# Kernel optimization log

Hardware: AMD Instinct MI355X
Metric: run time of the kernel (lower is better)

Reference implementation:

```python
import jax, jax.numpy as jnp
import numpy as np

N_USERS = 8192
D = 128
E = 262144        # known edges (nonzero_idx rows)
K = 131072        # static pad size for data-dependent candidate extraction
COS_THR = 0.3
TAU = 0.2


def setup_inputs() -> dict:
    key = jax.random.key(0)
    k1, k2, k3, k4 = jax.random.split(key, 4)
    user_emb = jax.random.normal(k1, (N_USERS, D), dtype=jnp.float32)
    nonzero_idx = jax.random.randint(k2, (E, 2), 0, N_USERS)
    W = jax.random.normal(k3, (2, 2 * D), dtype=jnp.float32) * 0.05  # mlp_s weight [2, 2*latent]
    b = jnp.zeros((2,), dtype=jnp.float32)                            # mlp_s bias
    gumbel_noise = jax.random.gumbel(k4, (E + K, 2), dtype=jnp.float32)
    return {"user_emb": user_emb, "W": W, "b": b,
            "gumbel_noise": gumbel_noise, "nonzero_idx": nonzero_idx}


def reference(user_emb, W, b, gumbel_noise, nonzero_idx):
    n = user_emb.shape[0]
    # ---- get_candidate_pair ----
    norm = jnp.linalg.norm(user_emb, axis=1, keepdims=True)
    u = user_emb / jnp.maximum(norm, 1e-12)          # F.normalize(dim=1)
    cos = u @ u.T                                    # [n, n]
    diag = jnp.arange(n)
    cos = cos.at[diag, diag].set(-1.0)               # fill_diagonal_(-1)
    cos = cos.at[nonzero_idx[:, 0], nonzero_idx[:, 1]].set(-1.0)
    mask = cos > COS_THR
    # static-size nonzero; padded slots point at (0,0) where cos == -1,
    # so they behave as invalid candidates (weight 0 downstream).
    ci, cj = jnp.nonzero(mask, size=K, fill_value=0)
    cand_vals = cos[ci, cj]                          # padded entries = -1
    cand_idx = jnp.stack([ci, cj], axis=1)           # [K, 2]

    # ---- forward ----
    pair_idx = jnp.concatenate([nonzero_idx, cand_idx], axis=0)   # [E+K, 2]
    u_emb = user_emb[pair_idx[:, 0]]
    v_emb = user_emb[pair_idx[:, 1]]
    concat_emb = jnp.concatenate([u_emb, v_emb], axis=1)          # [E+K, 2D]
    logits = concat_emb @ W.T + b                                 # [E+K, 2]

    # hard gumbel-softmax (straight-through)
    y_soft = jax.nn.softmax((logits + gumbel_noise) / TAU, axis=-1)
    y_hard = jax.nn.one_hot(jnp.argmax(y_soft, axis=-1), 2, dtype=y_soft.dtype)
    gumbel_output = y_hard + y_soft - jax.lax.stop_gradient(y_soft)
    gumbel_retain = gumbel_output[:, 0]                           # [E+K]

    # ---- get_edge_weight ----
    cand_w = jnp.maximum(cand_vals, 0.0)                          # masked_fill(<0, 0)
    weights = jnp.concatenate([jnp.ones((E,), dtype=cand_w.dtype), cand_w])
    w = gumbel_retain * weights                                   # [E+K]
    gumbel_01 = w
    gumbel_retain_w = jnp.concatenate([w[:, None], w[:, None]], axis=0)  # [2(E+K), 1]
    return gumbel_01, gumbel_retain_w, pair_idx
```

## Files before the change

kernel.cpp:

```cpp
#include <hip/hip_runtime.h>
#include <hip/hip_bf16.h>
#include <math.h>

#define N_USERS 8192
#define DIMS    128
#define EDGES   262144
#define KCAND   131072
#define NTOT    (EDGES + KCAND)
#define LISTCAP 131072
#define CAPB    1024
#define NTILES  1056
#define COS_THR 0.3f
#define EPS_SEL 6e-3f
#define LOGIT_MARGIN 2e-3f
#define DEADKEY 0xFFFFFFFFu

typedef short bf16x8 __attribute__((ext_vector_type(8)));
typedef float f32x4  __attribute__((ext_vector_type(4)));


__global__ __launch_bounds__(256) void prep_k(const float* __restrict__ x,
                                              const float* __restrict__ W,
                                              const int* __restrict__ nz,
                                              float* __restrict__ un,
                                              unsigned short* __restrict__ u0,
                                              float4* __restrict__ P,
                                              unsigned* __restrict__ excl) {
  if (blockIdx.x < 256) {
#pragma clang fp contract(off)
    const int tid  = threadIdx.x;
    const int rloc = tid >> 3;
    const int j    = tid & 7;
    const int i    = blockIdx.x * 32 + rloc;
    const float* r = x + (size_t)i * DIMS;

    float vals[16];
    float a = 0.f;
#pragma unroll
    for (int b8 = 0; b8 < 16; ++b8) {
      float t = r[b8 * 8 + j];
      vals[b8] = t;
      a = a + t * t;
    }
    a = a + __shfl_xor(a, 1, 64);
    a = a + __shfl_xor(a, 2, 64);
    float s = a + __shfl_xor(a, 4, 64);
    float n = (float)sqrt((double)s);
    n = fmaxf(n, 1e-12f);

    unsigned short* slab = u0 + (size_t)(i >> 7) * 16384 + (i & 127) * 8;
    float p0 = 0.f, p1 = 0.f, p2 = 0.f, p3 = 0.f;
#pragma unroll
    for (int b8 = 0; b8 < 16; ++b8) {
      int k = b8 * 8 + j;
      float t = vals[b8];
      float v = t / n;
      un[(size_t)i * DIMS + k] = v;
      __hip_bfloat16 h = __float2bfloat16(v);
      slab[(size_t)b8 * 1024 + j] = *(unsigned short*)&h;
      p0 = fmaf(t, W[k], p0);
      p1 = fmaf(t, W[128 + k], p1);
      p2 = fmaf(t, W[256 + k], p2);
      p3 = fmaf(t, W[384 + k], p3);
    }
#pragma unroll
    for (int m = 1; m < 8; m <<= 1) {
      p0 += __shfl_xor(p0, m, 64);
      p1 += __shfl_xor(p1, m, 64);
      p2 += __shfl_xor(p2, m, 64);
      p3 += __shfl_xor(p3, m, 64);
    }
    if (j == 0) P[i] = make_float4(p0, p1, p2, p3);
  } else {
    int t = (blockIdx.x - 256) * 256 + threadIdx.x;
    if (t < EDGES) {
      uint2 e = ((const uint2*)nz)[t];
      atomicOr(&excl[(size_t)e.x * 256 + (e.y >> 5)], 1u << (e.y & 31));
    }
  }
}

__global__ __launch_bounds__(512) void mfma_pass(const unsigned short* __restrict__ u0,
                                                 uint2* __restrict__ list,
                                                 int* __restrict__ gcount) {
  __shared__ uint2 svec[CAPB];
  __shared__ int lcnt, lbase;

  const int tid  = threadIdx.x;
  const int lane = tid & 63;
  const int wv   = tid >> 6;
  const int quad = lane >> 4;
  const int l15  = lane & 15;

  int b = blockIdx.x, cj = 0;
  while ((cj + 1) * (cj + 2) <= b) ++cj;
  const int ri = b - cj * (cj + 1);
  const int I0 = ri * 128, J0 = cj * 256;
  const int moff = (wv & 3) * 32;
  const int nhalf = wv >> 2;
  const int jbase = J0 + nhalf * 128;

  if (tid == 0) lcnt = 0;
  __syncthreads();

  const unsigned short* __restrict__ Abase = u0 + (size_t)ri * 16384;
  const unsigned short* __restrict__ Bbase = u0 + (size_t)(cj * 2 + nhalf) * 16384;

  f32x4 acc[2][8];
#pragma unroll
  for (int mt = 0; mt < 2; ++mt)
#pragma unroll
    for (int nt = 0; nt < 8; ++nt)
#pragma unroll
      for (int g = 0; g < 4; ++g) acc[mt][nt][g] = 0.f;

  bf16x8 a0_0, a0_1, b0_0, b0_1, b0_2, b0_3, b0_4, b0_5, b0_6, b0_7;
  bf16x8 a1_0, a1_1, b1_0, b1_1, b1_2, b1_3, b1_4, b1_5, b1_6, b1_7;

#define LOADF(AN0, AN1, BN0, BN1, BN2, BN3, BN4, BN5, BN6, BN7, KC)           \
  {                                                                           \
    const int cq = (KC) * 4 + quad;                                           \
    AN0 = *(const bf16x8*)&Abase[(size_t)(cq * 128 + moff + l15) * 8];        \
    AN1 = *(const bf16x8*)&Abase[(size_t)(cq * 128 + moff + 16 + l15) * 8];   \
    BN0 = *(const bf16x8*)&Bbase[(size_t)(cq * 128 + 0 * 16 + l15) * 8];      \
    BN1 = *(const bf16x8*)&Bbase[(size_t)(cq * 128 + 1 * 16 + l15) * 8];      \
    BN2 = *(const bf16x8*)&Bbase[(size_t)(cq * 128 + 2 * 16 + l15) * 8];      \
    BN3 = *(const bf16x8*)&Bbase[(size_t)(cq * 128 + 3 * 16 + l15) * 8];      \
    BN4 = *(const bf16x8*)&Bbase[(size_t)(cq * 128 + 4 * 16 + l15) * 8];      \
    BN5 = *(const bf16x8*)&Bbase[(size_t)(cq * 128 + 5 * 16 + l15) * 8];      \
    BN6 = *(const bf16x8*)&Bbase[(size_t)(cq * 128 + 6 * 16 + l15) * 8];      \
    BN7 = *(const bf16x8*)&Bbase[(size_t)(cq * 128 + 7 * 16 + l15) * 8];      \
  }

#define MFMAF(AN0, AN1, BN0, BN1, BN2, BN3, BN4, BN5, BN6, BN7)               \
  {                                                                           \
    acc[0][0] = __builtin_amdgcn_mfma_f32_16x16x32_bf16(AN0, BN0, acc[0][0], 0, 0, 0); \
    acc[0][1] = __builtin_amdgcn_mfma_f32_16x16x32_bf16(AN0, BN1, acc[0][1], 0, 0, 0); \
    acc[0][2] = __builtin_amdgcn_mfma_f32_16x16x32_bf16(AN0, BN2, acc[0][2], 0, 0, 0); \
    acc[0][3] = __builtin_amdgcn_mfma_f32_16x16x32_bf16(AN0, BN3, acc[0][3], 0, 0, 0); \
    acc[0][4] = __builtin_amdgcn_mfma_f32_16x16x32_bf16(AN0, BN4, acc[0][4], 0, 0, 0); \
    acc[0][5] = __builtin_amdgcn_mfma_f32_16x16x32_bf16(AN0, BN5, acc[0][5], 0, 0, 0); \
    acc[0][6] = __builtin_amdgcn_mfma_f32_16x16x32_bf16(AN0, BN6, acc[0][6], 0, 0, 0); \
    acc[0][7] = __builtin_amdgcn_mfma_f32_16x16x32_bf16(AN0, BN7, acc[0][7], 0, 0, 0); \
    acc[1][0] = __builtin_amdgcn_mfma_f32_16x16x32_bf16(AN1, BN0, acc[1][0], 0, 0, 0); \
    acc[1][1] = __builtin_amdgcn_mfma_f32_16x16x32_bf16(AN1, BN1, acc[1][1], 0, 0, 0); \
    acc[1][2] = __builtin_amdgcn_mfma_f32_16x16x32_bf16(AN1, BN2, acc[1][2], 0, 0, 0); \
    acc[1][3] = __builtin_amdgcn_mfma_f32_16x16x32_bf16(AN1, BN3, acc[1][3], 0, 0, 0); \
    acc[1][4] = __builtin_amdgcn_mfma_f32_16x16x32_bf16(AN1, BN4, acc[1][4], 0, 0, 0); \
    acc[1][5] = __builtin_amdgcn_mfma_f32_16x16x32_bf16(AN1, BN5, acc[1][5], 0, 0, 0); \
    acc[1][6] = __builtin_amdgcn_mfma_f32_16x16x32_bf16(AN1, BN6, acc[1][6], 0, 0, 0); \
    acc[1][7] = __builtin_amdgcn_mfma_f32_16x16x32_bf16(AN1, BN7, acc[1][7], 0, 0, 0); \
  }

  LOADF(a0_0, a0_1, b0_0, b0_1, b0_2, b0_3, b0_4, b0_5, b0_6, b0_7, 0)
  LOADF(a1_0, a1_1, b1_0, b1_1, b1_2, b1_3, b1_4, b1_5, b1_6, b1_7, 1)
  MFMAF(a0_0, a0_1, b0_0, b0_1, b0_2, b0_3, b0_4, b0_5, b0_6, b0_7)
  LOADF(a0_0, a0_1, b0_0, b0_1, b0_2, b0_3, b0_4, b0_5, b0_6, b0_7, 2)
  MFMAF(a1_0, a1_1, b1_0, b1_1, b1_2, b1_3, b1_4, b1_5, b1_6, b1_7)
  LOADF(a1_0, a1_1, b1_0, b1_1, b1_2, b1_3, b1_4, b1_5, b1_6, b1_7, 3)
  MFMAF(a0_0, a0_1, b0_0, b0_1, b0_2, b0_3, b0_4, b0_5, b0_6, b0_7)
  MFMAF(a1_0, a1_1, b1_0, b1_1, b1_2, b1_3, b1_4, b1_5, b1_6, b1_7)
#undef LOADF
#undef MFMAF

#pragma unroll
  for (int mt = 0; mt < 2; ++mt)
#pragma unroll
    for (int nt = 0; nt < 8; ++nt)
#pragma unroll
      for (int g = 0; g < 4; ++g) {
        float v = acc[mt][nt][g];
        if (v > COS_THR - EPS_SEL) {
          int i = I0 + moff + mt * 16 + quad * 4 + g;
          int j = jbase + nt * 16 + l15;
          if (j > i) {
            int idx = atomicAdd(&lcnt, 2);
            if (idx + 1 < CAPB) {
              svec[idx]     = make_uint2(((unsigned)i << 13) | j,
                                         __float_as_uint(v));
              svec[idx + 1] = make_uint2(((unsigned)j << 13) | i,
                                         __float_as_uint(v));
            }
          }
        }
      }

  __syncthreads();
  int n = min(lcnt, CAPB);
  if (tid == 0) lbase = atomicAdd(gcount, n);
  __syncthreads();
  int base = lbase;
  for (int t = tid; t < n; t += 512) {
    int o = base + t;
    if (o < LISTCAP) list[o] = svec[t];
  }
}

__global__ __launch_bounds__(256) void resolve_hist_k(const float* __restrict__ un,
                                                      const unsigned* __restrict__ excl,
                                                      uint2* __restrict__ list,
                                                      const int* __restrict__ gcount,
                                                      int* __restrict__ row_cnt) {
  int t = blockIdx.x * 256 + threadIdx.x;
  int n = min(*gcount, LISTCAP);
  if (t >= n) return;
  uint2 e = list[t];
  int i = e.x >> 13, j = e.x & 8191;
  unsigned word = excl[(size_t)i * 256 + (j >> 5)];
  bool alive = !((word >> (j & 31)) & 1u);
  float v = __uint_as_float(e.y);
  if (alive && v <= COS_THR + EPS_SEL) {
    const float* a = un + (size_t)i * DIMS;
    const float* b = un + (size_t)j * DIMS;
    float s = 0.f;
    for (int k = 0; k < DIMS; ++k) s = fmaf(a[k], b[k], s);
    alive = (s > COS_THR);
    if (alive) list[t] = make_uint2(e.x, __float_as_uint(s));
  }
  if (!alive) list[t] = make_uint2(DEADKEY, 0u);
  else        atomicAdd(&row_cnt[i], 1);
}

__global__ __launch_bounds__(256) void scan8k(const int* __restrict__ cnt,
                                              int* __restrict__ off) {
  __shared__ int sm[256];
  int t = threadIdx.x;
  int base = t * 32;
  int s = 0;
  for (int i = 0; i < 32; ++i) s += cnt[base + i];
  sm[t] = s;
  __syncthreads();
  int x = s;
  for (int d = 1; d < 256; d <<= 1) {
    int y = (t >= d) ? sm[t - d] : 0;
    __syncthreads();
    x += y;
    sm[t] = x;
    __syncthreads();
  }
  int run = x - s;
  for (int i = 0; i < 32; ++i) { off[base + i] = run; run += cnt[base + i]; }
  if (t == 255) off[N_USERS] = x;
}

__global__ __launch_bounds__(256) void scatter_k(const uint2* __restrict__ list,
                                                 const int* __restrict__ gcount,
                                                 const int* __restrict__ row_off,
                                                 int* __restrict__ row_pos,
                                                 int* __restrict__ cand_i,
                                                 int* __restrict__ cand_j,
                                                 float* __restrict__ cand_v) {
  int t = blockIdx.x * 256 + threadIdx.x;
  int n = min(*gcount, LISTCAP);
  if (t >= n) return;
  uint2 e = list[t];
  if (e.x == DEADKEY) return;
  int i = e.x >> 13, j = e.x & 8191;
  int pos = row_off[i] + atomicAdd(&row_pos[i], 1);
  if (pos < KCAND) {
    cand_i[pos] = i;
    cand_j[pos] = j;
    cand_v[pos] = __uint_as_float(e.y);
  }
}

__global__ __launch_bounds__(256) void sortrow_k(const int* __restrict__ row_off,
                                                 const int* __restrict__ row_cnt,
                                                 int* __restrict__ cand_j,
                                                 float* __restrict__ cand_v) {
  int r = blockIdx.x * 256 + threadIdx.x;
  if (r >= N_USERS) return;
  int o = row_off[r], c = row_cnt[r];
  if (o + c > KCAND) c = max(0, KCAND - o);
  for (int a = 1; a < c; ++a) {
    int jv = cand_j[o + a];
    float vv = cand_v[o + a];
    int b = a - 1;
    while (b >= 0 && cand_j[o + b] > jv) {
      cand_j[o + b + 1] = cand_j[o + b];
      cand_v[o + b + 1] = cand_v[o + b];
      --b;
    }
    cand_j[o + b + 1] = jv;
    cand_v[o + b + 1] = vv;
  }
}

__global__ __launch_bounds__(256) void finalize_k(const float* __restrict__ ue,
                                                  const float* __restrict__ W,
                                                  const float* __restrict__ b,
                                                  const float* __restrict__ g,
                                                  const int* __restrict__ nz,
                                                  const int* __restrict__ cand_i,
                                                  const int* __restrict__ cand_j,
                                                  const float* __restrict__ cand_v,
                                                  const int* __restrict__ row_off,
                                                  const float4* __restrict__ P,
                                                  float* __restrict__ out) {
  int p = blockIdx.x * 256 + threadIdx.x;
  if (p >= NTOT) return;

  int i, j;
  float wgt;
  if (p < EDGES) {
    i = nz[2 * p];
    j = nz[2 * p + 1];
    wgt = 1.0f;
  } else {
    int q = p - EDGES;
    if (q >= row_off[N_USERS]) {
      out[p] = 0.0f;
      out[NTOT + p] = 0.0f;
      out[2 * NTOT + p] = 0.0f;
      out[3 * NTOT + 2 * p + 0] = 0.0f;
      out[3 * NTOT + 2 * p + 1] = 0.0f;
      return;
    }
    i = cand_i[q];
    j = cand_j[q];
    wgt = fmaxf(cand_v[q], 0.0f);
  }

  float4 Pi = P[i], Pj = P[j];
  float l0 = Pi.x + Pj.y + b[0];
  float l1 = Pi.z + Pj.w + b[1];
  float g0 = g[2 * p], g1 = g[2 * p + 1];
  float s0 = l0 + g0, s1 = l1 + g1;

  if (fabsf(s0 - s1) < LOGIT_MARGIN) {
    const float* ri = ue + (size_t)i * DIMS;
    const float* rj = ue + (size_t)j * DIMS;
    float e0 = 0.f, e1 = 0.f;
    for (int k = 0; k < DIMS; ++k) {
      e0 = fmaf(ri[k], W[k], e0);
      e1 = fmaf(ri[k], W[256 + k], e1);
    }
    for (int k = 0; k < DIMS; ++k) {
      e0 = fmaf(rj[k], W[128 + k], e0);
      e1 = fmaf(rj[k], W[384 + k], e1);
    }
    s0 = (e0 + b[0]) + g0;
    s1 = (e1 + b[1]) + g1;
  }

  float w = (s0 >= s1) ? wgt : 0.0f;

  out[p] = w;
  out[NTOT + p] = w;
  out[2 * NTOT + p] = w;
  out[3 * NTOT + 2 * p + 0] = (float)i;
  out[3 * NTOT + 2 * p + 1] = (float)j;
}

extern "C" void kernel_launch(void* const* d_in, const int* in_sizes, int n_in,
                              void* d_out, int out_size, void* d_ws, size_t ws_size,
                              hipStream_t stream) {
  (void)in_sizes; (void)n_in; (void)out_size; (void)ws_size;

  const float* user_emb = (const float*)d_in[0];
  const float* W        = (const float*)d_in[1];
  const float* b        = (const float*)d_in[2];
  const float* gnoise   = (const float*)d_in[3];
  const int*   nz       = (const int*)d_in[4];
  float* out = (float*)d_out;

  char* ws = (char*)d_ws;
  float*          un      = (float*)(ws + 0);
  unsigned short* u0      = (unsigned short*)(ws + (4u << 20));
  unsigned*       excl    = (unsigned*)(ws + (6u << 20));
  char*           zbase   = ws + (14u << 20);
  int*            gcount  = (int*)(zbase);
  int*            row_cnt = (int*)(zbase + 64);
  int*            row_pos = (int*)(zbase + 64 + 32768);
  int*            row_off = (int*)(ws + (14u << 20) + (96u << 10));
  uint2*          list    = (uint2*)(ws + (15u << 20));
  int*            cand_i  = (int*)(ws + (16u << 20));
  int*            cand_j  = (int*)(ws + (16u << 20) + (512u << 10));
  float*          cand_v  = (float*)(ws + (17u << 20));
  float4*         P       = (float4*)(ws + (17u << 20) + (512u << 10));

  hipMemsetAsync(excl, 0, (8u << 20) + (96u << 10), stream);

  prep_k<<<256 + EDGES / 256, 256, 0, stream>>>(user_emb, W, nz, un, u0, P, excl);
  mfma_pass<<<NTILES, 512, 0, stream>>>(u0, list, gcount);
  resolve_hist_k<<<LISTCAP / 256, 256, 0, stream>>>(un, excl, list, gcount,
                                                    row_cnt);
  scan8k<<<1, 256, 0, stream>>>(row_cnt, row_off);
  scatter_k<<<LISTCAP / 256, 256, 0, stream>>>(list, gcount, row_off, row_pos,
                                               cand_i, cand_j, cand_v);
  sortrow_k<<<N_USERS / 256, 256, 0, stream>>>(row_off, row_cnt, cand_j, cand_v);
  finalize_k<<<NTOT / 256, 256, 0, stream>>>(user_emb, W, b, gnoise, nz,
                                             cand_i, cand_j, cand_v, row_off,
                                             P, out);
}
```

Measured before the change: 148.5 us.

## Fuse candidate resolve into MFMA pass and merge scan/scatter/sort/finalize into one kernel

The exclusion-bitmap check, exact fp32 recheck of near-threshold pairs and per-row counting move into the MFMA tile epilogue, so the separate resolve kernel is gone. Scan, scatter, per-row insertion sort and output emission are merged into a single 256-block tail kernel. Each block redundantly recomputes the global prefix scan over row counts and scans the whole candidate list to pick out its own 32 rows. The goal is fewer launches and fewer global round trips, at the cost of redundant per-block list scans and serialized dot products inside the MFMA epilogue.

```diff
diff --git a/kernel.cpp b/kernel.cpp
--- a/kernel.cpp
+++ b/kernel.cpp
@@ -13,11 +13,17 @@
 #define COS_THR 0.3f
 #define EPS_SEL 6e-3f
 #define LOGIT_MARGIN 2e-3f
-#define DEADKEY 0xFFFFFFFFu
 
 typedef short bf16x8 __attribute__((ext_vector_type(8)));
 typedef float f32x4  __attribute__((ext_vector_type(4)));
 
+
+__attribute__((noinline)) __device__ float exact_dot(const float* __restrict__ a,
+                                                     const float* __restrict__ b) {
+  float s = 0.f;
+  for (int k = 0; k < DIMS; ++k) s = fmaf(a[k], b[k], s);
+  return s;
+}
 
 __global__ __launch_bounds__(256) void prep_k(const float* __restrict__ x,
                                               const float* __restrict__ W,
@@ -81,8 +87,11 @@
 }
 
 __global__ __launch_bounds__(512) void mfma_pass(const unsigned short* __restrict__ u0,
+                                                 const float* __restrict__ un,
+                                                 const unsigned* __restrict__ excl,
                                                  uint2* __restrict__ list,
-                                                 int* __restrict__ gcount) {
+                                                 int* __restrict__ gcount,
+                                                 int* __restrict__ row_cnt) {
   __shared__ uint2 svec[CAPB];
   __shared__ int lcnt, lbase;
 
@@ -174,12 +183,30 @@
           int i = I0 + moff + mt * 16 + quad * 4 + g;
           int j = jbase + nt * 16 + l15;
           if (j > i) {
-            int idx = atomicAdd(&lcnt, 2);
-            if (idx + 1 < CAPB) {
-              svec[idx]     = make_uint2(((unsigned)i << 13) | j,
-                                         __float_as_uint(v));
-              svec[idx + 1] = make_uint2(((unsigned)j << 13) | i,
-                                         __float_as_uint(v));
+            float vv = v;
+            bool pass = true;
+            if (v <= COS_THR + EPS_SEL) {
+              vv = exact_dot(un + (size_t)i * DIMS, un + (size_t)j * DIMS);
+              pass = (vv > COS_THR);
+            }
+            if (pass) {
+              unsigned wij = excl[(size_t)i * 256 + (j >> 5)];
+              unsigned wji = excl[(size_t)j * 256 + (i >> 5)];
+              unsigned uvv = __float_as_uint(vv);
+              if (!((wij >> (j & 31)) & 1u)) {
+                int idx = atomicAdd(&lcnt, 1);
+                if (idx < CAPB) {
+                  svec[idx] = make_uint2(((unsigned)i << 13) | j, uvv);
+                  atomicAdd(&row_cnt[i], 1);
+                }
+              }
+              if (!((wji >> (i & 31)) & 1u)) {
+                int idx = atomicAdd(&lcnt, 1);
+                if (idx < CAPB) {
+                  svec[idx] = make_uint2(((unsigned)j << 13) | i, uvv);
+                  atomicAdd(&row_cnt[j], 1);
+                }
+              }
             }
           }
         }
@@ -196,131 +223,13 @@
   }
 }
 
-__global__ __launch_bounds__(256) void resolve_hist_k(const float* __restrict__ un,
-                                                      const unsigned* __restrict__ excl,
-                                                      uint2* __restrict__ list,
-                                                      const int* __restrict__ gcount,
-                                                      int* __restrict__ row_cnt) {
-  int t = blockIdx.x * 256 + threadIdx.x;
-  int n = min(*gcount, LISTCAP);
-  if (t >= n) return;
-  uint2 e = list[t];
-  int i = e.x >> 13, j = e.x & 8191;
-  unsigned word = excl[(size_t)i * 256 + (j >> 5)];
-  bool alive = !((word >> (j & 31)) & 1u);
-  float v = __uint_as_float(e.y);
-  if (alive && v <= COS_THR + EPS_SEL) {
-    const float* a = un + (size_t)i * DIMS;
-    const float* b = un + (size_t)j * DIMS;
-    float s = 0.f;
-    for (int k = 0; k < DIMS; ++k) s = fmaf(a[k], b[k], s);
-    alive = (s > COS_THR);
-    if (alive) list[t] = make_uint2(e.x, __float_as_uint(s));
-  }
-  if (!alive) list[t] = make_uint2(DEADKEY, 0u);
-  else        atomicAdd(&row_cnt[i], 1);
-}
-
-__global__ __launch_bounds__(256) void scan8k(const int* __restrict__ cnt,
-                                              int* __restrict__ off) {
-  __shared__ int sm[256];
-  int t = threadIdx.x;
-  int base = t * 32;
-  int s = 0;
-  for (int i = 0; i < 32; ++i) s += cnt[base + i];
-  sm[t] = s;
-  __syncthreads();
-  int x = s;
-  for (int d = 1; d < 256; d <<= 1) {
-    int y = (t >= d) ? sm[t - d] : 0;
-    __syncthreads();
-    x += y;
-    sm[t] = x;
-    __syncthreads();
-  }
-  int run = x - s;
-  for (int i = 0; i < 32; ++i) { off[base + i] = run; run += cnt[base + i]; }
-  if (t == 255) off[N_USERS] = x;
-}
-
-__global__ __launch_bounds__(256) void scatter_k(const uint2* __restrict__ list,
-                                                 const int* __restrict__ gcount,
-                                                 const int* __restrict__ row_off,
-                                                 int* __restrict__ row_pos,
-                                                 int* __restrict__ cand_i,
-                                                 int* __restrict__ cand_j,
-                                                 float* __restrict__ cand_v) {
-  int t = blockIdx.x * 256 + threadIdx.x;
-  int n = min(*gcount, LISTCAP);
-  if (t >= n) return;
-  uint2 e = list[t];
-  if (e.x == DEADKEY) return;
-  int i = e.x >> 13, j = e.x & 8191;
-  int pos = row_off[i] + atomicAdd(&row_pos[i], 1);
-  if (pos < KCAND) {
-    cand_i[pos] = i;
-    cand_j[pos] = j;
-    cand_v[pos] = __uint_as_float(e.y);
-  }
-}
-
-__global__ __launch_bounds__(256) void sortrow_k(const int* __restrict__ row_off,
-                                                 const int* __restrict__ row_cnt,
-                                                 int* __restrict__ cand_j,
-                                                 float* __restrict__ cand_v) {
-  int r = blockIdx.x * 256 + threadIdx.x;
-  if (r >= N_USERS) return;
-  int o = row_off[r], c = row_cnt[r];
-  if (o + c > KCAND) c = max(0, KCAND - o);
-  for (int a = 1; a < c; ++a) {
-    int jv = cand_j[o + a];
-    float vv = cand_v[o + a];
-    int b = a - 1;
-    while (b >= 0 && cand_j[o + b] > jv) {
-      cand_j[o + b + 1] = cand_j[o + b];
-      cand_v[o + b + 1] = cand_v[o + b];
-      --b;
-    }
-    cand_j[o + b + 1] = jv;
-    cand_v[o + b + 1] = vv;
-  }
-}
-
-__global__ __launch_bounds__(256) void finalize_k(const float* __restrict__ ue,
-                                                  const float* __restrict__ W,
-                                                  const float* __restrict__ b,
-                                                  const float* __restrict__ g,
-                                                  const int* __restrict__ nz,
-                                                  const int* __restrict__ cand_i,
-                                                  const int* __restrict__ cand_j,
-                                                  const float* __restrict__ cand_v,
-                                                  const int* __restrict__ row_off,
-                                                  const float4* __restrict__ P,
-                                                  float* __restrict__ out) {
-  int p = blockIdx.x * 256 + threadIdx.x;
-  if (p >= NTOT) return;
-
-  int i, j;
-  float wgt;
-  if (p < EDGES) {
-    i = nz[2 * p];
-    j = nz[2 * p + 1];
-    wgt = 1.0f;
-  } else {
-    int q = p - EDGES;
-    if (q >= row_off[N_USERS]) {
-      out[p] = 0.0f;
-      out[NTOT + p] = 0.0f;
-      out[2 * NTOT + p] = 0.0f;
-      out[3 * NTOT + 2 * p + 0] = 0.0f;
-      out[3 * NTOT + 2 * p + 1] = 0.0f;
-      return;
-    }
-    i = cand_i[q];
-    j = cand_j[q];
-    wgt = fmaxf(cand_v[q], 0.0f);
-  }
-
+__device__ __forceinline__ void emit_out(int p, int i, int j, float wgt,
+                                         const float4* __restrict__ P,
+                                         const float* __restrict__ b,
+                                         const float* __restrict__ g,
+                                         const float* __restrict__ ue,
+                                         const float* __restrict__ W,
+                                         float* __restrict__ out) {
   float4 Pi = P[i], Pj = P[j];
   float l0 = Pi.x + Pj.y + b[0];
   float l1 = Pi.z + Pj.w + b[1];
@@ -344,12 +253,121 @@
   }
 
   float w = (s0 >= s1) ? wgt : 0.0f;
-
   out[p] = w;
   out[NTOT + p] = w;
   out[2 * NTOT + p] = w;
   out[3 * NTOT + 2 * p + 0] = (float)i;
   out[3 * NTOT + 2 * p + 1] = (float)j;
+}
+
+__global__ __launch_bounds__(256) void tail_k(const uint2* __restrict__ list,
+                                              const int* __restrict__ gcount,
+                                              const int* __restrict__ row_cnt,
+                                              int* __restrict__ cand_i,
+                                              int* __restrict__ cand_j,
+                                              float* __restrict__ cand_v,
+                                              const float* __restrict__ ue,
+                                              const float* __restrict__ W,
+                                              const float* __restrict__ b,
+                                              const float* __restrict__ g,
+                                              const int* __restrict__ nz,
+                                              const float4* __restrict__ P,
+                                              float* __restrict__ out) {
+  __shared__ int s_chunk[256];
+  __shared__ int s_off[32];
+  __shared__ int s_pos[32];
+  __shared__ int s_lo, s_M;
+
+  const int tid = threadIdx.x;
+  const int bo  = blockIdx.x;
+
+  int s = 0;
+  {
+    const int rb = tid * 32;
+    for (int k = 0; k < 32; ++k) s += row_cnt[rb + k];
+  }
+  s_chunk[tid] = s;
+  __syncthreads();
+  int x = s;
+  for (int d = 1; d < 256; d <<= 1) {
+    int y = (tid >= d) ? s_chunk[tid - d] : 0;
+    __syncthreads();
+    x += y;
+    s_chunk[tid] = x;
+    __syncthreads();
+  }
+  if (tid == 255) s_M = x;
+  if (tid == bo)  s_lo = x - s;
+  __syncthreads();
+  if (tid == 0) {
+    int run = s_lo;
+    for (int k = 0; k < 32; ++k) {
+      s_off[k] = run;
+      run += row_cnt[bo * 32 + k];
+    }
+  }
+  if (tid < 32) s_pos[tid] = 0;
+  __syncthreads();
+
+  const int n = min(*gcount, LISTCAP);
+  const int M = s_M;
+
+  for (int t = tid; t < n; t += 256) {
+    uint2 e = list[t];
+    int i = e.x >> 13;
+    if ((i >> 5) == bo) {
+      int lr = i & 31;
+      int pos = s_off[lr] + atomicAdd(&s_pos[lr], 1);
+      if (pos < KCAND) {
+        cand_i[pos] = i;
+        cand_j[pos] = e.x & 8191;
+        cand_v[pos] = __uint_as_float(e.y);
+      }
+    }
+  }
+  __syncthreads();
+
+  if (tid < 32) {
+    int o = s_off[tid], c = s_pos[tid];
+    if (o + c > KCAND) c = max(0, KCAND - o);
+    for (int a = 1; a < c; ++a) {
+      int jv = cand_j[o + a];
+      float vv = cand_v[o + a];
+      int bq = a - 1;
+      while (bq >= 0 && cand_j[o + bq] > jv) {
+        cand_j[o + bq + 1] = cand_j[o + bq];
+        cand_v[o + bq + 1] = cand_v[o + bq];
+        --bq;
+      }
+      cand_j[o + bq + 1] = jv;
+      cand_v[o + bq + 1] = vv;
+    }
+  }
+  __syncthreads();
+
+  {
+    int lo = s_off[0];
+    int hi = min(s_off[31] + s_pos[31], KCAND);
+    for (int q = lo + tid; q < hi; q += 256) {
+      int ci = cand_i[q], cjj = cand_j[q];
+      float wgt = fmaxf(cand_v[q], 0.0f);
+      emit_out(EDGES + q, ci, cjj, wgt, P, b, g, ue, W, out);
+    }
+  }
+
+  for (int p = bo * 1024 + tid; p < bo * 1024 + 1024; p += 256) {
+    uint2 e = ((const uint2*)nz)[p];
+    emit_out(p, (int)e.x, (int)e.y, 1.0f, P, b, g, ue, W, out);
+  }
+
+  for (int q = M + bo * 256 + tid; q < KCAND; q += 256 * 256) {
+    int p = EDGES + q;
+    out[p] = 0.0f;
+    out[NTOT + p] = 0.0f;
+    out[2 * NTOT + p] = 0.0f;
+    out[3 * NTOT + 2 * p + 0] = 0.0f;
+    out[3 * NTOT + 2 * p + 1] = 0.0f;
+  }
 }
 
 extern "C" void kernel_launch(void* const* d_in, const int* in_sizes, int n_in,
@@ -371,8 +389,6 @@
   char*           zbase   = ws + (14u << 20);
   int*            gcount  = (int*)(zbase);
   int*            row_cnt = (int*)(zbase + 64);
-  int*            row_pos = (int*)(zbase + 64 + 32768);
-  int*            row_off = (int*)(ws + (14u << 20) + (96u << 10));
   uint2*          list    = (uint2*)(ws + (15u << 20));
   int*            cand_i  = (int*)(ws + (16u << 20));
   int*            cand_j  = (int*)(ws + (16u << 20) + (512u << 10));
@@ -382,14 +398,7 @@
   hipMemsetAsync(excl, 0, (8u << 20) + (96u << 10), stream);
 
   prep_k<<<256 + EDGES / 256, 256, 0, stream>>>(user_emb, W, nz, un, u0, P, excl);
-  mfma_pass<<<NTILES, 512, 0, stream>>>(u0, list, gcount);
-  resolve_hist_k<<<LISTCAP / 256, 256, 0, stream>>>(un, excl, list, gcount,
-                                                    row_cnt);
-  scan8k<<<1, 256, 0, stream>>>(row_cnt, row_off);
-  scatter_k<<<LISTCAP / 256, 256, 0, stream>>>(list, gcount, row_off, row_pos,
-                                               cand_i, cand_j, cand_v);
-  sortrow_k<<<N_USERS / 256, 256, 0, stream>>>(row_off, row_cnt, cand_j, cand_v);
-  finalize_k<<<NTOT / 256, 256, 0, stream>>>(user_emb, W, b, gnoise, nz,
-                                             cand_i, cand_j, cand_v, row_off,
-                                             P, out);
-}
+  mfma_pass<<<NTILES, 512, 0, stream>>>(u0, un, excl, list, gcount, row_cnt);
+  tail_k<<<256, 256, 0, stream>>>(list, gcount, row_cnt, cand_i, cand_j, cand_v,
+                                  user_emb, W, b, gnoise, nz, P, out);
+}
```

Result: slower. 181.3 us (+22.2%).
